# Optimization experiments

Measured on AMD Instinct MI355X. Metric: run time of the kernel, lower is better.

The kernel has to match this reference:

```python
import jax, jax.numpy as jnp
import numpy as np


def setup_inputs() -> dict:
    key = jax.random.key(0)
    k1, k2, k3 = jax.random.split(key, 3)
    B, L, Z, C = 2048, 128, 256, 256  # predictive_steps == L
    z = jax.random.normal(k1, (B, L, Z), dtype=jnp.float32)
    c = jax.random.normal(k2, (B, L, C), dtype=jnp.float32)
    # original inits trans to zeros; use small random values so output is non-trivial
    trans = jax.random.normal(k3, (L, Z, C), dtype=jnp.float32) * 0.02
    return {"z": z, "c": c, "trans": trans}


def reference(z, c, trans):
    # Original per-t: r[:, t] = (z[:, t] @ trans[t] @ c[:, t].T).sum(-1)
    # Row-sum of the (b x b) score matrix equals projecting z onto trans[t] @ sum_b c[b, t],
    # which is exactly the same math without materializing the (b x b) intermediate.
    csum = jnp.sum(c, axis=0)                      # (L, C)
    v = jnp.einsum('lzc,lc->lz', trans, csum)      # (L, Z)
    r = jnp.einsum('blz,lz->bl', z, v)             # (B, L)
    return jnp.exp(r)
```

## Files before the change

### kernel.cpp

```cpp
#include <hip/hip_runtime.h>
#include <math.h>

#define NB 2048
#define NL 128
#define NZ 256
#define NC 256
#define BCHUNK 128
#define NCHUNK (NB / BCHUNK)

__global__ __launch_bounds__(256) void zero_kernel(float* __restrict__ p, int n) {
    int i = blockIdx.x * blockDim.x + threadIdx.x;
    if (i < n) p[i] = 0.0f;
}

__global__ __launch_bounds__(256) void csum_kernel(const float* __restrict__ c,
                                                   float* __restrict__ csum) {
    const int l     = blockIdx.x;
    const int chunk = blockIdx.y;
    const int lane  = threadIdx.x & 63;
    const int w     = threadIdx.x >> 6;

    const size_t b0 = (size_t)chunk * BCHUNK + (size_t)w * (BCHUNK / 4);
    const float4* base = (const float4*)(c + (b0 * NL + l) * NC) + lane;

    float4 acc = {0.f, 0.f, 0.f, 0.f};
#pragma unroll 8
    for (int i = 0; i < BCHUNK / 4; ++i) {
        float4 t = base[(size_t)i * (NL * NC / 4)];
        acc.x += t.x; acc.y += t.y; acc.z += t.z; acc.w += t.w;
    }

    __shared__ float4 s4[256];
    s4[threadIdx.x] = acc;
    __syncthreads();

    if (threadIdx.x < 64) {
        float4 a = s4[threadIdx.x];
        float4 b = s4[64 + threadIdx.x];
        float4 d = s4[128 + threadIdx.x];
        float4 e = s4[192 + threadIdx.x];
        float* dst = csum + l * NC + threadIdx.x * 4;
        atomicAdd(dst + 0, a.x + b.x + d.x + e.x);
        atomicAdd(dst + 1, a.y + b.y + d.y + e.y);
        atomicAdd(dst + 2, a.z + b.z + d.z + e.z);
        atomicAdd(dst + 3, a.w + b.w + d.w + e.w);
    }
}

__global__ __launch_bounds__(256) void v_kernel(const float* __restrict__ trans,
                                                const float* __restrict__ csum,
                                                float* __restrict__ v) {
    const int lane = threadIdx.x & 63;
    const int wv   = threadIdx.x >> 6;
    const int o    = blockIdx.x * 4 + wv;
    const int l    = o >> 8;

    float4 t = ((const float4*)(trans + (size_t)o * NC))[lane];
    float4 s = ((const float4*)(csum + l * NC))[lane];
    float acc = t.x * s.x + t.y * s.y + t.z * s.z + t.w * s.w;

#pragma unroll
    for (int m = 32; m >= 1; m >>= 1) acc += __shfl_xor(acc, m, 64);
    if (lane == 0) v[o] = acc;
}

__global__ __launch_bounds__(256) void r_kernel(const float* __restrict__ z,
                                                const float* __restrict__ v,
                                                float* __restrict__ out) {
    const int lane = threadIdx.x & 63;
    const int wv   = threadIdx.x >> 6;
    const int o    = blockIdx.x * 4 + wv;
    const int l    = o & (NL - 1);

    float4 zf = ((const float4*)(z + (size_t)o * NZ))[lane];
    float4 vf = ((const float4*)(v + l * NZ))[lane];
    float acc = zf.x * vf.x + zf.y * vf.y + zf.z * vf.z + zf.w * vf.w;

#pragma unroll
    for (int m = 32; m >= 1; m >>= 1) acc += __shfl_xor(acc, m, 64);
    if (lane == 0) out[o] = expf(fminf(acc, 88.0f));
}

extern "C" void kernel_launch(void* const* d_in, const int* in_sizes, int n_in,
                              void* d_out, int out_size, void* d_ws, size_t ws_size,
                              hipStream_t stream) {
    const float* z     = (const float*)d_in[0];
    const float* c     = (const float*)d_in[1];
    const float* trans = (const float*)d_in[2];
    float* out = (float*)d_out;

    float* csum = (float*)d_ws;
    float* v    = csum + NL * NC;

    zero_kernel<<<(NL * NC + 255) / 256, 256, 0, stream>>>(csum, NL * NC);

    dim3 gA(NL, NCHUNK);
    csum_kernel<<<gA, 256, 0, stream>>>(c, csum);

    v_kernel<<<(NL * NZ) / 4, 256, 0, stream>>>(trans, csum, v);

    r_kernel<<<(NB * NL) / 4, 256, 0, stream>>>(z, v, out);
}
```

Measured before the change: 528.9 us.

## Replace atomic csum with two-stage reduction and batch rows per wave

```diff
diff --git a/kernel.cpp b/kernel.cpp
--- a/kernel.cpp
+++ b/kernel.cpp
@@ -8,13 +8,8 @@
 #define BCHUNK 128
 #define NCHUNK (NB / BCHUNK)
 
-__global__ __launch_bounds__(256) void zero_kernel(float* __restrict__ p, int n) {
-    int i = blockIdx.x * blockDim.x + threadIdx.x;
-    if (i < n) p[i] = 0.0f;
-}
-
-__global__ __launch_bounds__(256) void csum_kernel(const float* __restrict__ c,
-                                                   float* __restrict__ csum) {
+__global__ __launch_bounds__(256) void csum_partial_kernel(const float* __restrict__ c,
+                                                           float* __restrict__ partial) {
     const int l     = blockIdx.x;
     const int chunk = blockIdx.y;
     const int lane  = threadIdx.x & 63;
@@ -39,12 +34,24 @@
         float4 b = s4[64 + threadIdx.x];
         float4 d = s4[128 + threadIdx.x];
         float4 e = s4[192 + threadIdx.x];
-        float* dst = csum + l * NC + threadIdx.x * 4;
-        atomicAdd(dst + 0, a.x + b.x + d.x + e.x);
-        atomicAdd(dst + 1, a.y + b.y + d.y + e.y);
-        atomicAdd(dst + 2, a.z + b.z + d.z + e.z);
-        atomicAdd(dst + 3, a.w + b.w + d.w + e.w);
+        float4 r;
+        r.x = a.x + b.x + d.x + e.x;
+        r.y = a.y + b.y + d.y + e.y;
+        r.z = a.z + b.z + d.z + e.z;
+        r.w = a.w + b.w + d.w + e.w;
+        ((float4*)(partial + ((size_t)chunk * NL + l) * NC))[threadIdx.x] = r;
     }
+}
+
+__global__ __launch_bounds__(256) void csum_reduce_kernel(const float* __restrict__ partial,
+                                                          float* __restrict__ csum) {
+    const int l = blockIdx.x;
+    const int t = threadIdx.x;
+    float s = 0.f;
+#pragma unroll
+    for (int k = 0; k < NCHUNK; ++k)
+        s += partial[((size_t)k * NL + l) * NC + t];
+    csum[l * NC + t] = s;
 }
 
 __global__ __launch_bounds__(256) void v_kernel(const float* __restrict__ trans,
@@ -52,16 +59,23 @@
                                                 float* __restrict__ v) {
     const int lane = threadIdx.x & 63;
     const int wv   = threadIdx.x >> 6;
-    const int o    = blockIdx.x * 4 + wv;
-    const int l    = o >> 8;
+    const int o0   = (blockIdx.x * 4 + wv) * 4;
+    const int l    = o0 >> 8;
 
-    float4 t = ((const float4*)(trans + (size_t)o * NC))[lane];
     float4 s = ((const float4*)(csum + l * NC))[lane];
-    float acc = t.x * s.x + t.y * s.y + t.z * s.z + t.w * s.w;
 
+    float acc[4];
 #pragma unroll
-    for (int m = 32; m >= 1; m >>= 1) acc += __shfl_xor(acc, m, 64);
-    if (lane == 0) v[o] = acc;
+    for (int k = 0; k < 4; ++k) {
+        float4 t = ((const float4*)(trans + (size_t)(o0 + k) * NC))[lane];
+        acc[k] = t.x * s.x + t.y * s.y + t.z * s.z + t.w * s.w;
+    }
+#pragma unroll
+    for (int m = 32; m >= 1; m >>= 1) {
+#pragma unroll
+        for (int k = 0; k < 4; ++k) acc[k] += __shfl_xor(acc[k], m, 64);
+    }
+    if (lane == 0) *((float4*)(v + o0)) = make_float4(acc[0], acc[1], acc[2], acc[3]);
 }
 
 __global__ __launch_bounds__(256) void r_kernel(const float* __restrict__ z,
@@ -69,16 +83,32 @@
                                                 float* __restrict__ out) {
     const int lane = threadIdx.x & 63;
     const int wv   = threadIdx.x >> 6;
-    const int o    = blockIdx.x * 4 + wv;
-    const int l    = o & (NL - 1);
-
-    float4 zf = ((const float4*)(z + (size_t)o * NZ))[lane];
-    float4 vf = ((const float4*)(v + l * NZ))[lane];
-    float acc = zf.x * vf.x + zf.y * vf.y + zf.z * vf.z + zf.w * vf.w;
+    const int gw   = blockIdx.x * 4 + wv;
 
 #pragma unroll
-    for (int m = 32; m >= 1; m >>= 1) acc += __shfl_xor(acc, m, 64);
-    if (lane == 0) out[o] = expf(fminf(acc, 88.0f));
+    for (int jj = 0; jj < 4; ++jj) {
+        const int o0 = gw * 16 + jj * 4;
+        float acc[4];
+#pragma unroll
+        for (int k = 0; k < 4; ++k) {
+            const int o = o0 + k;
+            const int l = o & (NL - 1);
+            float4 zf = ((const float4*)(z + (size_t)o * NZ))[lane];
+            float4 vf = ((const float4*)(v + l * NZ))[lane];
+            acc[k] = zf.x * vf.x + zf.y * vf.y + zf.z * vf.z + zf.w * vf.w;
+        }
+#pragma unroll
+        for (int m = 32; m >= 1; m >>= 1) {
+#pragma unroll
+            for (int k = 0; k < 4; ++k) acc[k] += __shfl_xor(acc[k], m, 64);
+        }
+        if (lane == 0) {
+            *((float4*)(out + o0)) = make_float4(expf(fminf(acc[0], 88.f)),
+                                                 expf(fminf(acc[1], 88.f)),
+                                                 expf(fminf(acc[2], 88.f)),
+                                                 expf(fminf(acc[3], 88.f)));
+        }
+    }
 }
 
 extern "C" void kernel_launch(void* const* d_in, const int* in_sizes, int n_in,
@@ -89,15 +119,16 @@
     const float* trans = (const float*)d_in[2];
     float* out = (float*)d_out;
 
-    float* csum = (float*)d_ws;
-    float* v    = csum + NL * NC;
-
-    zero_kernel<<<(NL * NC + 255) / 256, 256, 0, stream>>>(csum, NL * NC);
+    float* partial = (float*)d_ws;
+    float* csum    = partial + (size_t)NCHUNK * NL * NC;
+    float* v       = csum + NL * NC;
 
     dim3 gA(NL, NCHUNK);
-    csum_kernel<<<gA, 256, 0, stream>>>(c, csum);
+    csum_partial_kernel<<<gA, 256, 0, stream>>>(c, partial);
 
-    v_kernel<<<(NL * NZ) / 4, 256, 0, stream>>>(trans, csum, v);
+    csum_reduce_kernel<<<NL, 256, 0, stream>>>(partial, csum);
 
-    r_kernel<<<(NB * NL) / 4, 256, 0, stream>>>(z, v, out);
+    v_kernel<<<(NL * NZ) / 16, 256, 0, stream>>>(trans, csum, v);
+
+    r_kernel<<<(NB * NL) / 64, 256, 0, stream>>>(z, v, out);
 }
```

Result: no change. 525.6 us (-0.6%).
